# Kernel optimization log

Measured on AMD Instinct MI355X. Metric: run time of the kernel, lower is better.

Reference implementation:

```python
import jax, jax.numpy as jnp
import numpy as np

B, P, C, WIN = 64, 24, 40, 64          # batch, acoustic params, phoneme classes, window
L1 = WIN - 4                            # after conv k=5: 60
L2 = L1 - 4                             # after primary conv k=5: 56
R = P * L2                              # num_routes = 24*56 = 1344
IC, OC = 32, 16                         # capsule in/out channels
NUM_ITERS = 3


def squash(x, axis=-1):
    sq = jnp.sum(x * x, axis=axis, keepdims=True)
    return (sq / (1.0 + sq)) * x / (jnp.sqrt(sq) + 1e-8)


def conv1d(x, w, b):
    # x: (B, Cin, L), w: (Cout, Cin, K)
    out = jax.lax.conv_general_dilated(x, w, (1,), 'VALID',
                                       dimension_numbers=('NCH', 'OIH', 'NCH'))
    return out + b[None, :, None]


def batchnorm(x, g, b):
    # training-mode BN over (batch, length) per channel; x: (B, Ch, L)
    m = jnp.mean(x, axis=(0, 2), keepdims=True)
    v = jnp.var(x, axis=(0, 2), keepdims=True)
    return g[None, :, None] * (x - m) / jnp.sqrt(v + 1e-5) + b[None, :, None]


def setup_inputs() -> dict:
    key = jax.random.key(0)
    ks = jax.random.split(key, 12)
    d = {}
    d['x'] = jax.random.normal(ks[0], (B, WIN, P), dtype=jnp.float32)
    # project: Conv1d(24 -> 256, k=5) + BN(256)
    d['conv1_w'] = jax.random.normal(ks[1], (256, P, 5), dtype=jnp.float32) * (1.0 / np.sqrt(P * 5))
    d['conv1_b'] = jnp.zeros((256,), dtype=jnp.float32)
    d['bn1_g'] = jnp.ones((256,), dtype=jnp.float32)
    d['bn1_b'] = jnp.zeros((256,), dtype=jnp.float32)
    d['prim_w'] = jax.random.normal(ks[2], (P * 32, 256, 5), dtype=jnp.float32) * (1.0 / np.sqrt(256 * 5))
    d['prim_b'] = jnp.zeros((P * 32,), dtype=jnp.float32)
    d['bn2_g'] = jnp.ones((32,), dtype=jnp.float32)
    d['bn2_b'] = jnp.zeros((32,), dtype=jnp.float32)
    # digit capsule routing weights (1, C, R, 16, 32) as in torch (randn)
    d['W_cap'] = jax.random.normal(ks[3], (1, C, R, OC, IC), dtype=jnp.float32) * 0.05
    # classifier: Linear(16*C -> 256), Linear(256 -> C)
    d['cls_w1'] = jax.random.normal(ks[4], (256, OC * C), dtype=jnp.float32) * (1.0 / np.sqrt(OC * C))
    d['cls_b1'] = jnp.zeros((256,), dtype=jnp.float32)
    d['cls_w2'] = jax.random.normal(ks[5], (C, 256), dtype=jnp.float32) * (1.0 / np.sqrt(256))
    d['cls_b2'] = jnp.zeros((C,), dtype=jnp.float32)
    d['dec_w1'] = jax.random.normal(ks[6], (256, OC * C), dtype=jnp.float32) * (1.0 / np.sqrt(OC * C))
    d['dec_b1'] = jnp.zeros((256,), dtype=jnp.float32)
    d['dec_w2'] = jax.random.normal(ks[7], (WIN * P, 256), dtype=jnp.float32) * (1.0 / np.sqrt(256))
    d['dec_b2'] = jnp.zeros((WIN * P,), dtype=jnp.float32)
    return d


def reference(x, conv1_w, conv1_b, bn1_g, bn1_b, prim_w, prim_b, bn2_g, bn2_b,
              W_cap, cls_w1, cls_b1, cls_w2, cls_b2, dec_w1, dec_b1, dec_w2, dec_b2):
    h = jax.nn.relu(batchnorm(conv1d(jnp.transpose(x, (0, 2, 1)), conv1_w, conv1_b), bn1_g, bn1_b))
    # primary capsules: fused conv -> (B, 24*32, 56); capsule i occupies length slice i
    u = conv1d(h, prim_w, prim_b)                       # (B, 768, 56)
    u = u.reshape(B, P, 32, L2).transpose(0, 2, 1, 3).reshape(B, 32, R)  # concat along length dim
    u = batchnorm(u, bn2_g, bn2_b)
    u = squash(jnp.transpose(u, (0, 2, 1)), axis=-1)    # (B, R, 32)
    # digit capsule: u_hat = W @ x  -> (B, C, R, 16)
    u_hat = jnp.einsum('crdi,bri->bcrd', W_cap[0], u)
    # dynamic routing
    b_ij = jnp.zeros((B, C, R, 1), dtype=u_hat.dtype)
    for it in range(NUM_ITERS):
        c_ij = jax.nn.softmax(b_ij, axis=1)             # softmax over capsules
        s_j = jnp.sum(c_ij * u_hat, axis=2)             # (B, C, 16)
        v_j = squash(s_j, axis=-1)
        if it < NUM_ITERS - 1:
            a_ij = jnp.einsum('bcrd,bcd->bcr', u_hat, v_j)[..., None]
            b_ij = b_ij + a_ij
    flat = v_j.reshape(B, -1)                           # (B, 640)
    logits = jax.nn.relu(flat @ cls_w1.T + cls_b1) @ cls_w2.T + cls_b2
    pred_y = jax.nn.softmax(logits, axis=-1)
    # y is None branch: one-hot of argmax
    y = jax.nn.one_hot(jnp.argmax(pred_y, axis=1), C, dtype=v_j.dtype)
    masked = (v_j * y[:, :, None]).reshape(B, -1)
    pred_x = jax.nn.sigmoid(jax.nn.relu(masked @ dec_w1.T + dec_b1) @ dec_w2.T + dec_b2)
    pred_x = pred_x.reshape(B, WIN, P)
    return (pred_x, pred_y)
```

## Files before the change

kernel.cpp:

```cpp
#include <hip/hip_runtime.h>
#include <math.h>

#define BB_ 64
#define P_  24
#define C_  40
#define WIN_ 64
#define L1_ 60
#define L2_ 56
#define R_  1344

#define O_USQ   0ull
#define O_UHAT  2752512ull
#define O_H     30277632ull
#define O_HB    3735552ull
#define O_WT    4227072ull
#define O_UP    25755648ull
#define O_HID   31260672ull
#define O_HD    31277056ull
#define O_STATS 57802752ull
#define O_A1    57803328ull
#define O_B1S   57803584ull
#define O_A2    57803840ull
#define O_B2S   57803872ull
#define O_S     57803904ull
#define O_V     57967744ull
#define WS_FLOATS_NEEDED 58008704ull

typedef short bf16x8 __attribute__((ext_vector_type(8)));
typedef float f32x4 __attribute__((ext_vector_type(4)));

__device__ __forceinline__ float dot4f(float4 a, float4 b) {
    return a.x*b.x + a.y*b.y + a.z*b.z + a.w*b.w;
}

__device__ __forceinline__ unsigned short f2bf(float x) {
    unsigned int u = __float_as_uint(x);
    u += 0x7fffu + ((u >> 16) & 1u);
    return (unsigned short)(u >> 16);
}
__device__ __forceinline__ float bfl(unsigned int u) {
    return __uint_as_float(u << 16);
}
__device__ __forceinline__ float bfh(unsigned int u) {
    return __uint_as_float(u & 0xffff0000u);
}

__global__ void k0w(const float* __restrict__ w2, unsigned short* __restrict__ wt) {
    int o2 = blockIdx.x, t = threadIdx.x;
    const float* src = &w2[(size_t)o2 * 1280 + t * 5];
    #pragma unroll
    for (int kt = 0; kt < 5; kt++)
        wt[((size_t)kt * 768 + o2) * 256 + t] = f2bf(src[kt]);
}

__global__ void k1_conv1(const float* __restrict__ x, const float* __restrict__ w1,
                         const float* __restrict__ c1b, float* __restrict__ h) {
    __shared__ float xs[24 * 20];
    __shared__ float wl[64 * 121];
    int t = threadIdx.x;
    int lq = blockIdx.x, b = blockIdx.y, ocg = blockIdx.z;
    for (int idx = t; idx < 456; idx += 256) {
        int p = idx / 19, tau = idx - p * 19;
        xs[p * 20 + tau] = x[b * 1536 + (lq * 15 + tau) * 24 + p];
    }
    for (int idx = t; idx < 7680; idx += 256) {
        int o_ = idx / 120, cix = idx - o_ * 120;
        wl[o_ * 121 + cix] = w1[(ocg * 64 + o_) * 120 + cix];
    }
    __syncthreads();
    int g = t >> 6;
    int ol = t & 63;
    int LV = (g < 3) ? 4 : 3;
    int o = ocg * 64 + ol;
    float acc[4] = {0.f, 0.f, 0.f, 0.f};
    for (int p = 0; p < 24; p++) {
        float4 xa = *(const float4*)&xs[p * 20 + g * 4];
        float4 xb = *(const float4*)&xs[p * 20 + g * 4 + 4];
        float xr[8] = {xa.x, xa.y, xa.z, xa.w, xb.x, xb.y, xb.z, xb.w};
        #pragma unroll
        for (int k = 0; k < 5; k++) {
            float w = wl[ol * 121 + p * 5 + k];
            #pragma unroll
            for (int li = 0; li < 4; li++) acc[li] += xr[li + k] * w;
        }
    }
    for (int li = 0; li < LV; li++) {
        int l = lq * 15 + g * 4 + li;
        h[(size_t)(b * 60 + l) * 256 + o] = acc[li] + c1b[o];
    }
}

__global__ void k2a(const float* __restrict__ h, float* __restrict__ sum1, float* __restrict__ ss1) {
    int t = threadIdx.x;
    float s = 0.f, q = 0.f;
    for (int i = 0; i < 64; i++) {
        float v = h[(size_t)(blockIdx.x * 64 + i) * 256 + t];
        s += v; q += v * v;
    }
    atomicAdd(&sum1[t], s);
    atomicAdd(&ss1[t], q);
}

__global__ void k2b(const float* __restrict__ sum1, const float* __restrict__ ss1,
                    const float* __restrict__ g, const float* __restrict__ be,
                    float* __restrict__ a1, float* __restrict__ b1s) {
    int o = threadIdx.x;
    float m = sum1[o] * (1.f / 3840.f);
    float v = ss1[o] * (1.f / 3840.f) - m * m;
    float a = g[o] / sqrtf(v + 1e-5f);
    a1[o] = a;
    b1s[o] = be[o] - m * a;
}

__global__ void k2c(const float* __restrict__ h, const float* __restrict__ a1,
                    const float* __restrict__ b1s, unsigned short* __restrict__ hb) {
    int gid = blockIdx.x * 256 + threadIdx.x;
    int base = gid * 4;
    int ic = base & 255;
    float4 v = *(const float4*)&h[base];
    float4 a = *(const float4*)&a1[ic];
    float4 bb = *(const float4*)&b1s[ic];
    unsigned int w0 = (unsigned int)f2bf(fmaxf(v.x * a.x + bb.x, 0.f))
                    | ((unsigned int)f2bf(fmaxf(v.y * a.y + bb.y, 0.f)) << 16);
    unsigned int w1 = (unsigned int)f2bf(fmaxf(v.z * a.z + bb.z, 0.f))
                    | ((unsigned int)f2bf(fmaxf(v.w * a.w + bb.w, 0.f)) << 16);
    uint2 o = {w0, w1};
    *(uint2*)&hb[base] = o;
}

__global__ __launch_bounds__(256) void k3_mfma(
        const unsigned short* __restrict__ hb, const unsigned short* __restrict__ wt,
        const float* __restrict__ pb, float* __restrict__ up) {
    __shared__ unsigned short hs[68 * 40];
    __shared__ unsigned short wsd[5 * 64 * 40];
    int t = threadIdx.x;
    int m0 = blockIdx.x * 64;
    int b = blockIdx.y;
    int wid = t >> 6, lane = t & 63;
    int wm = wid >> 1, wn = wid & 1;
    int ln = lane & 15, grp = lane >> 4;

    f32x4 acc[2][2];
    #pragma unroll
    for (int i = 0; i < 2; i++)
        #pragma unroll
        for (int j = 0; j < 2; j++) acc[i][j] = (f32x4){0.f, 0.f, 0.f, 0.f};

    for (int ic0 = 0; ic0 < 256; ic0 += 32) {
        __syncthreads();
        for (int idx = t; idx < 272; idx += 256) {
            int row = idx >> 2, q = idx & 3;
            int hrow = row < 60 ? row : 59;
            uint4 v = *(const uint4*)&hb[((size_t)b * 60 + hrow) * 256 + ic0 + q * 8];
            *(uint4*)&hs[row * 40 + q * 8] = v;
        }
        #pragma unroll
        for (int it = 0; it < 5; it++) {
            int idx = it * 256 + t;
            int row = idx >> 2, q = idx & 3;
            int kt = row >> 6, o2l = row & 63;
            uint4 v = *(const uint4*)&wt[((size_t)kt * 768 + m0 + o2l) * 256 + ic0 + q * 8];
            *(uint4*)&wsd[row * 40 + q * 8] = v;
        }
        __syncthreads();
        #pragma unroll
        for (int kt = 0; kt < 5; kt++) {
            bf16x8 af0 = *(const bf16x8*)&wsd[(kt * 64 + wm * 32 + ln) * 40 + grp * 8];
            bf16x8 af1 = *(const bf16x8*)&wsd[(kt * 64 + wm * 32 + 16 + ln) * 40 + grp * 8];
            bf16x8 bf0 = *(const bf16x8*)&hs[(wn * 32 + ln + kt) * 40 + grp * 8];
            bf16x8 bf1 = *(const bf16x8*)&hs[(wn * 32 + 16 + ln + kt) * 40 + grp * 8];
            acc[0][0] = __builtin_amdgcn_mfma_f32_16x16x32_bf16(af0, bf0, acc[0][0], 0, 0, 0);
            acc[0][1] = __builtin_amdgcn_mfma_f32_16x16x32_bf16(af0, bf1, acc[0][1], 0, 0, 0);
            acc[1][0] = __builtin_amdgcn_mfma_f32_16x16x32_bf16(af1, bf0, acc[1][0], 0, 0, 0);
            acc[1][1] = __builtin_amdgcn_mfma_f32_16x16x32_bf16(af1, bf1, acc[1][1], 0, 0, 0);
        }
    }
    #pragma unroll
    for (int ms = 0; ms < 2; ms++) {
        int o2 = m0 + wm * 32 + ms * 16 + grp * 4;
        float4 pv = *(const float4*)&pb[o2];
        #pragma unroll
        for (int ns = 0; ns < 2; ns++) {
            int l = wn * 32 + ns * 16 + ln;
            if (l < 56) {
                float4 v;
                v.x = acc[ms][ns][0] + pv.x;
                v.y = acc[ms][ns][1] + pv.y;
                v.z = acc[ms][ns][2] + pv.z;
                v.w = acc[ms][ns][3] + pv.w;
                *(float4*)&up[(size_t)b * 43008 + (size_t)l * 768 + o2] = v;
            }
        }
    }
}

__global__ void k4s(const float* __restrict__ up, float* __restrict__ sum2, float* __restrict__ ss2) {
    __shared__ float rs[256], rq[256];
    int t = threadIdx.x;
    float s = 0.f, q = 0.f;
    for (int i = 0; i < 32; i++) {
        size_t row = (size_t)(blockIdx.x * 32 + i) * 768;
        for (int c0 = 0; c0 < 768; c0 += 256) {
            float v = up[row + c0 + t];
            s += v; q += v * v;
        }
    }
    rs[t] = s; rq[t] = q;
    __syncthreads();
    if (t < 32) {
        float S = 0.f, Q = 0.f;
        for (int g2 = 0; g2 < 8; g2++) { S += rs[t + 32 * g2]; Q += rq[t + 32 * g2]; }
        atomicAdd(&sum2[t], S);
        atomicAdd(&ss2[t], Q);
    }
}

__global__ void k4b(const float* __restrict__ sum2, const float* __restrict__ ss2,
                    const float* __restrict__ g, const float* __restrict__ be,
                    float* __restrict__ a2, float* __restrict__ b2s) {
    int j = threadIdx.x;
    if (j >= 32) return;
    float m = sum2[j] * (1.f / 86016.f);
    float v = ss2[j] * (1.f / 86016.f) - m * m;
    float a = g[j] / sqrtf(v + 1e-5f);
    a2[j] = a;
    b2s[j] = be[j] - m * a;
}

__global__ void k5(const float* __restrict__ up, const float* __restrict__ a2,
                   const float* __restrict__ b2s, float* __restrict__ usq) {
    int t = threadIdx.x;
    int row = blockIdx.x * 8 + (t >> 5);
    int j = t & 31;
    int b = row / 1344, r = row - b * 1344;
    int p = r / 56, l = r - p * 56;
    float v = up[(size_t)b * 43008 + (size_t)l * 768 + p * 32 + j];
    float xv = a2[j] * v + b2s[j];
    float sq = xv * xv;
    #pragma unroll
    for (int m = 16; m >= 1; m >>= 1) sq += __shfl_xor(sq, m, 32);
    float scale = (sq / (1.f + sq)) / (sqrtf(sq) + 1e-8f);
    usq[(size_t)row * 32 + j] = xv * scale;
}

__global__ __launch_bounds__(256) void k6_uhat(const float* __restrict__ usq,
                                               const float* __restrict__ W,
                                               unsigned short* __restrict__ uhb) {
    __shared__ float us[64 * 36];
    __shared__ float wl[128 * 36];
    int t = threadIdx.x;
    int cdt = blockIdx.x, r = blockIdx.y;

    #pragma unroll
    for (int q = 0; q < 2; q++) {
        int idx4 = q * 256 + t;
        int b = idx4 >> 3, i4 = idx4 & 7;
        float4 v = *(const float4*)&usq[(size_t)(b * 1344 + r) * 32 + i4 * 4];
        *(float4*)&us[b * 36 + i4 * 4] = v;
    }
    #pragma unroll
    for (int q = 0; q < 4; q++) {
        int idx4 = q * 256 + t;
        int c_l = idx4 >> 7;
        int rest4 = idx4 & 127;
        float4 v = *(const float4*)&W[(size_t)(cdt * 8 + c_l) * 688128ull +
                                      (size_t)r * 512 + rest4 * 4];
        int cd_l = c_l * 16 + (rest4 >> 3);
        int i4 = rest4 & 7;
        *(float4*)&wl[cd_l * 36 + i4 * 4] = v;
    }
    __syncthreads();

    int tb = t & 7, tcd = t >> 3;
    float acc[8][4];
    #pragma unroll
    for (int i = 0; i < 8; i++)
        #pragma unroll
        for (int j = 0; j < 4; j++) acc[i][j] = 0.f;

    #pragma unroll
    for (int k4 = 0; k4 < 8; k4++) {
        float4 wv[4], ub[8];
        #pragma unroll
        for (int j = 0; j < 4; j++)
            wv[j] = *(const float4*)&wl[(tcd * 4 + j) * 36 + k4 * 4];
        #pragma unroll
        for (int bj = 0; bj < 8; bj++)
            ub[bj] = *(const float4*)&us[(bj * 8 + tb) * 36 + k4 * 4];
        #pragma unroll
        for (int bj = 0; bj < 8; bj++)
            #pragma unroll
            for (int j = 0; j < 4; j++)
                acc[bj][j] += dot4f(ub[bj], wv[j]);
    }

    #pragma unroll
    for (int bj = 0; bj < 8; bj++) {
        int b = bj * 8 + tb;
        unsigned int lo = (unsigned int)f2bf(acc[bj][0]) | ((unsigned int)f2bf(acc[bj][1]) << 16);
        unsigned int hi = (unsigned int)f2bf(acc[bj][2]) | ((unsigned int)f2bf(acc[bj][3]) << 16);
        uint2 o = {lo, hi};
        *(uint2*)&uhb[(size_t)(b * 1344 + r) * 640 + cdt * 128 + tcd * 4] = o;
    }
}

template<int UNIFORM>
__global__ void k_route(const unsigned short* __restrict__ uhb, const float* __restrict__ vsum,
                        float* __restrict__ sout) {
    __shared__ float sl[2560];
    int t = threadIdx.x, wid = t >> 6, lane = t & 63;
    int b = blockIdx.y, rt = blockIdx.x;
    bool act = lane < 40;
    int c = act ? lane : 0;
    float4 vs0 = {0,0,0,0}, vs1 = vs0, vs2 = vs0, vs3 = vs0;
    if (UNIFORM == 0 && act) {
        const float4* vp = (const float4*)&vsum[b * 640 + c * 16];
        vs0 = vp[0]; vs1 = vp[1]; vs2 = vp[2]; vs3 = vp[3];
    }
    float4 ac0 = {0,0,0,0}, ac1 = ac0, ac2 = ac0, ac3 = ac0;
    for (int i = 0; i < 8; i++) {
        int r = rt * 32 + wid * 8 + i;
        const uint4* u4 = (const uint4*)&uhb[((size_t)(b * 1344 + r) * 40 + c) * 16];
        float4 a0 = {0,0,0,0}, a1 = a0, a2 = a0, a3 = a0;
        if (act) {
            uint4 q0 = u4[0], q1 = u4[1];
            a0.x = bfl(q0.x); a0.y = bfh(q0.x); a0.z = bfl(q0.y); a0.w = bfh(q0.y);
            a1.x = bfl(q0.z); a1.y = bfh(q0.z); a1.z = bfl(q0.w); a1.w = bfh(q0.w);
            a2.x = bfl(q1.x); a2.y = bfh(q1.x); a2.z = bfl(q1.y); a2.w = bfh(q1.y);
            a3.x = bfl(q1.z); a3.y = bfh(q1.z); a3.z = bfl(q1.w); a3.w = bfh(q1.w);
        }
        float w;
        if (UNIFORM) {
            w = 0.025f;
        } else {
            float dt = act ? (dot4f(a0, vs0) + dot4f(a1, vs1) + dot4f(a2, vs2) + dot4f(a3, vs3))
                           : -1e30f;
            float mx = dt;
            #pragma unroll
            for (int m2 = 32; m2 >= 1; m2 >>= 1) mx = fmaxf(mx, __shfl_xor(mx, m2));
            float e = act ? __expf(dt - mx) : 0.f;
            float se = e;
            #pragma unroll
            for (int m2 = 32; m2 >= 1; m2 >>= 1) se += __shfl_xor(se, m2);
            w = e / se;
        }
        ac0.x += w * a0.x; ac0.y += w * a0.y; ac0.z += w * a0.z; ac0.w += w * a0.w;
        ac1.x += w * a1.x; ac1.y += w * a1.y; ac1.z += w * a1.z; ac1.w += w * a1.w;
        ac2.x += w * a2.x; ac2.y += w * a2.y; ac2.z += w * a2.z; ac2.w += w * a2.w;
        ac3.x += w * a3.x; ac3.y += w * a3.y; ac3.z += w * a3.z; ac3.w += w * a3.w;
    }
    if (act) {
        float4* sp = (float4*)&sl[wid * 640 + c * 16];
        sp[0] = ac0; sp[1] = ac1; sp[2] = ac2; sp[3] = ac3;
    }
    __syncthreads();
    for (int jj = t; jj < 640; jj += 256)
        atomicAdd(&sout[b * 640 + jj], sl[jj] + sl[640 + jj] + sl[1280 + jj] + sl[1920 + jj]);
}

__global__ void k8(const float* __restrict__ sin, float* __restrict__ vout,
                   float* __restrict__ vsum, int addsum) {
    int t = threadIdx.x;
    int row = blockIdx.x * 16 + (t >> 4);
    int d = t & 15;
    float v = sin[row * 16 + d];
    float sq = v * v;
    #pragma unroll
    for (int m = 8; m >= 1; m >>= 1) sq += __shfl_xor(sq, m, 16);
    float scale = (sq / (1.f + sq)) / (sqrtf(sq) + 1e-8f);
    float o = v * scale;
    vout[row * 16 + d] = o;
    if (addsum) vsum[row * 16 + d] += o;
}

__global__ void k10a(const float* __restrict__ v, const float* __restrict__ cw1,
                     const float* __restrict__ cb1, float* __restrict__ hid) {
    __shared__ float flat[640];
    int t = threadIdx.x;
    int b = blockIdx.x, hq = blockIdx.y;
    for (int j = t; j < 640; j += 256) flat[j] = v[b * 640 + j];
    __syncthreads();
    int h_l = t >> 2, s = t & 3;
    int h = hq * 64 + h_l;
    const float4* wr = (const float4*)&cw1[(size_t)h * 640 + s * 160];
    float a = 0.f;
    #pragma unroll
    for (int u = 0; u < 40; u++) {
        float4 w4 = wr[u];
        float4 f4 = *(const float4*)&flat[s * 160 + u * 4];
        a += dot4f(w4, f4);
    }
    a += __shfl_xor(a, 1);
    a += __shfl_xor(a, 2);
    if (s == 0) hid[b * 256 + h] = fmaxf(a + cb1[h], 0.f);
}

__global__ void k10bc(const float* __restrict__ v, const float* __restrict__ hid,
                      const float* __restrict__ cw2, const float* __restrict__ cb2,
                      const float* __restrict__ dw1, const float* __restrict__ db1,
                      float* __restrict__ out, float* __restrict__ hd) {
    __shared__ float hl[256], lgs[40], msk[16];
    __shared__ float smx, ssum;
    __shared__ int chat;
    int t = threadIdx.x, b = blockIdx.x;
    if (t < 256) hl[t] = hid[b * 256 + t];
    __syncthreads();
    {
        int c = t >> 3, s = t & 7;
        float p = 0.f;
        const float4* w4 = (const float4*)&cw2[c * 256 + s * 32];
        const float4* h4 = (const float4*)&hl[s * 32];
        #pragma unroll
        for (int u = 0; u < 8; u++) p += dot4f(w4[u], h4[u]);
        p += __shfl_xor(p, 1); p += __shfl_xor(p, 2); p += __shfl_xor(p, 4);
        if (s == 0) lgs[c] = p + cb2[c];
    }
    __syncthreads();
    if (t == 0) {
        float mx = lgs[0]; int am = 0;
        for (int c2 = 1; c2 < 40; c2++) if (lgs[c2] > mx) { mx = lgs[c2]; am = c2; }
        float se = 0.f;
        for (int c2 = 0; c2 < 40; c2++) se += __expf(lgs[c2] - mx);
        smx = mx; ssum = se; chat = am;
    }
    __syncthreads();
    if (t < 40) out[98304 + b * 40 + t] = __expf(lgs[t] - smx) / ssum;
    if (t < 16) msk[t] = v[b * 640 + chat * 16 + t];
    __syncthreads();
    if (t < 256) {
        int cb = chat * 16;
        float ad = db1[t];
        const float4* w4 = (const float4*)&dw1[(size_t)t * 640 + cb];
        #pragma unroll
        for (int u = 0; u < 4; u++) {
            float4 m4 = *(const float4*)&msk[u * 4];
            ad += dot4f(w4[u], m4);
        }
        hd[b * 256 + t] = fmaxf(ad, 0.f);
    }
}

__global__ void k10d(const float* __restrict__ hd, const float* __restrict__ dw2,
                     const float* __restrict__ db2, float* __restrict__ out) {
    __shared__ float hl[256];
    int t = threadIdx.x;
    int b = blockIdx.x, ot = blockIdx.y;
    if (t < 256) hl[t] = hd[b * 256 + t];
    __syncthreads();
    int o_l = t >> 2, s = t & 3;
    int o = ot * 64 + o_l;
    const float4* w4 = (const float4*)&dw2[(size_t)o * 256 + s * 64];
    const float4* h4 = (const float4*)&hl[s * 64];
    float z = 0.f;
    #pragma unroll
    for (int u = 0; u < 16; u++) z += dot4f(w4[u], h4[u]);
    z += __shfl_xor(z, 1);
    z += __shfl_xor(z, 2);
    if (s == 0) out[b * 1536 + o] = 1.f / (1.f + __expf(-(z + db2[o])));
}

extern "C" void kernel_launch(void* const* d_in, const int* in_sizes, int n_in,
                              void* d_out, int out_size, void* d_ws, size_t ws_size,
                              hipStream_t stream) {
    const float* x   = (const float*)d_in[0];
    const float* c1w = (const float*)d_in[1];
    const float* c1b = (const float*)d_in[2];
    const float* g1  = (const float*)d_in[3];
    const float* be1 = (const float*)d_in[4];
    const float* pw  = (const float*)d_in[5];
    const float* pb  = (const float*)d_in[6];
    const float* g2  = (const float*)d_in[7];
    const float* be2 = (const float*)d_in[8];
    const float* Wc  = (const float*)d_in[9];
    const float* cw1 = (const float*)d_in[10];
    const float* cb1 = (const float*)d_in[11];
    const float* cw2 = (const float*)d_in[12];
    const float* cb2 = (const float*)d_in[13];
    const float* dw1 = (const float*)d_in[14];
    const float* db1 = (const float*)d_in[15];
    const float* dw2 = (const float*)d_in[16];
    const float* db2 = (const float*)d_in[17];

    if (ws_size < WS_FLOATS_NEEDED * 4ull) return;

    float* ws  = (float*)d_ws;
    float* out = (float*)d_out;
    float* usq  = ws + O_USQ;
    unsigned short* uhb = (unsigned short*)(ws + O_UHAT);
    float* hpre = ws + O_H;
    unsigned short* hbb = (unsigned short*)(ws + O_HB);
    unsigned short* wtb = (unsigned short*)(ws + O_WT);
    float* up   = ws + O_UP;
    float* hidb = ws + O_HID;
    float* hdb  = ws + O_HD;
    float* sum1 = ws + O_STATS;
    float* ss1  = sum1 + 256;
    float* sum2 = ss1 + 256;
    float* ss2  = sum2 + 32;
    float* a1  = ws + O_A1;
    float* b1s = ws + O_B1S;
    float* a2  = ws + O_A2;
    float* b2s = ws + O_B2S;
    float* s0   = ws + O_S;
    float* s1   = s0 + 40960;
    float* s2   = s1 + 40960;
    float* vsum = s2 + 40960;
    float* vbuf = ws + O_V;

    hipMemsetAsync(sum1, 0, 576 * sizeof(float), stream);
    hipMemsetAsync(s0, 0, 163840 * sizeof(float), stream);

    k0w<<<768, 256, 0, stream>>>(pw, wtb);
    k1_conv1<<<dim3(4, 64, 4), 256, 0, stream>>>(x, c1w, c1b, hpre);
    k2a<<<60, 256, 0, stream>>>(hpre, sum1, ss1);
    k2b<<<1, 256, 0, stream>>>(sum1, ss1, g1, be1, a1, b1s);
    k2c<<<960, 256, 0, stream>>>(hpre, a1, b1s, hbb);
    k3_mfma<<<dim3(12, 64), 256, 0, stream>>>(hbb, wtb, pb, up);
    k4s<<<112, 256, 0, stream>>>(up, sum2, ss2);
    k4b<<<1, 64, 0, stream>>>(sum2, ss2, g2, be2, a2, b2s);
    k5<<<10752, 256, 0, stream>>>(up, a2, b2s, usq);
    k6_uhat<<<dim3(5, 1344), 256, 0, stream>>>(usq, Wc, uhb);
    k_route<1><<<dim3(42, 64), 256, 0, stream>>>(uhb, nullptr, s0);
    k8<<<160, 256, 0, stream>>>(s0, vbuf, vsum, 1);
    k_route<0><<<dim3(42, 64), 256, 0, stream>>>(uhb, vsum, s1);
    k8<<<160, 256, 0, stream>>>(s1, vbuf, vsum, 1);
    k_route<0><<<dim3(42, 64), 256, 0, stream>>>(uhb, vsum, s2);
    k8<<<160, 256, 0, stream>>>(s2, vbuf, vsum, 0);
    k10a<<<dim3(64, 4), 256, 0, stream>>>(vbuf, cw1, cb1, hidb);
    k10bc<<<64, 320, 0, stream>>>(vbuf, hidb, cw2, cb2, dw1, db1, out, hdb);
    k10d<<<dim3(64, 24), 256, 0, stream>>>(hdb, dw2, db2, out);
}
```

Before: 381.5 us.

## Compute u_hat with bf16 MFMA instead of scalar FP32 dot products

Replaces the FP32 FMA-based u_hat kernel with one that converts the capsule inputs and routing weights to bf16 and uses 16x16x32 MFMA instructions, with one block per route covering all 40 classes. W is read straight from global into registers with no LDS staging, and the capsule inputs are staged once in LDS as bf16. This cuts ALU work and shared-memory traffic. In exchange it adds bf16 rounding of the weights and inputs, which lowers precision.

```diff
diff --git a/kernel.cpp b/kernel.cpp
--- a/kernel.cpp
+++ b/kernel.cpp
@@ -243,64 +243,56 @@
     usq[(size_t)row * 32 + j] = xv * scale;
 }
 
-__global__ __launch_bounds__(256) void k6_uhat(const float* __restrict__ usq,
+__global__ __launch_bounds__(256) void k6_mfma(const float* __restrict__ usq,
                                                const float* __restrict__ W,
                                                unsigned short* __restrict__ uhb) {
-    __shared__ float us[64 * 36];
-    __shared__ float wl[128 * 36];
-    int t = threadIdx.x;
-    int cdt = blockIdx.x, r = blockIdx.y;
-
-    #pragma unroll
-    for (int q = 0; q < 2; q++) {
-        int idx4 = q * 256 + t;
-        int b = idx4 >> 3, i4 = idx4 & 7;
-        float4 v = *(const float4*)&usq[(size_t)(b * 1344 + r) * 32 + i4 * 4];
-        *(float4*)&us[b * 36 + i4 * 4] = v;
-    }
-    #pragma unroll
-    for (int q = 0; q < 4; q++) {
-        int idx4 = q * 256 + t;
-        int c_l = idx4 >> 7;
-        int rest4 = idx4 & 127;
-        float4 v = *(const float4*)&W[(size_t)(cdt * 8 + c_l) * 688128ull +
-                                      (size_t)r * 512 + rest4 * 4];
-        int cd_l = c_l * 16 + (rest4 >> 3);
-        int i4 = rest4 & 7;
-        *(float4*)&wl[cd_l * 36 + i4 * 4] = v;
-    }
-    __syncthreads();
-
-    int tb = t & 7, tcd = t >> 3;
-    float acc[8][4];
-    #pragma unroll
-    for (int i = 0; i < 8; i++)
-        #pragma unroll
-        for (int j = 0; j < 4; j++) acc[i][j] = 0.f;
-
-    #pragma unroll
-    for (int k4 = 0; k4 < 8; k4++) {
-        float4 wv[4], ub[8];
-        #pragma unroll
-        for (int j = 0; j < 4; j++)
-            wv[j] = *(const float4*)&wl[(tcd * 4 + j) * 36 + k4 * 4];
-        #pragma unroll
-        for (int bj = 0; bj < 8; bj++)
-            ub[bj] = *(const float4*)&us[(bj * 8 + tb) * 36 + k4 * 4];
-        #pragma unroll
-        for (int bj = 0; bj < 8; bj++)
-            #pragma unroll
-            for (int j = 0; j < 4; j++)
-                acc[bj][j] += dot4f(ub[bj], wv[j]);
-    }
-
-    #pragma unroll
-    for (int bj = 0; bj < 8; bj++) {
-        int b = bj * 8 + tb;
-        unsigned int lo = (unsigned int)f2bf(acc[bj][0]) | ((unsigned int)f2bf(acc[bj][1]) << 16);
-        unsigned int hi = (unsigned int)f2bf(acc[bj][2]) | ((unsigned int)f2bf(acc[bj][3]) << 16);
-        uint2 o = {lo, hi};
-        *(uint2*)&uhb[(size_t)(b * 1344 + r) * 640 + cdt * 128 + tcd * 4] = o;
+    __shared__ unsigned short ub[64 * 40];
+    int t = threadIdx.x;
+    int r = blockIdx.x;
+    {
+        int b = t >> 2, ch = t & 3;
+        const float* src = &usq[((size_t)b * 1344 + r) * 32 + ch * 8];
+        float4 v0 = *(const float4*)&src[0];
+        float4 v1 = *(const float4*)&src[4];
+        uint4 pk;
+        pk.x = (unsigned)f2bf(v0.x) | ((unsigned)f2bf(v0.y) << 16);
+        pk.y = (unsigned)f2bf(v0.z) | ((unsigned)f2bf(v0.w) << 16);
+        pk.z = (unsigned)f2bf(v1.x) | ((unsigned)f2bf(v1.y) << 16);
+        pk.w = (unsigned)f2bf(v1.z) | ((unsigned)f2bf(v1.w) << 16);
+        *(uint4*)&ub[b * 40 + ch * 8] = pk;
+    }
+    __syncthreads();
+    int w = t >> 6, lane = t & 63;
+    int ln = lane & 15, g = lane >> 4;
+    bf16x8 bfr[4];
+    #pragma unroll
+    for (int nt = 0; nt < 4; nt++)
+        bfr[nt] = *(const bf16x8*)&ub[(nt * 16 + ln) * 40 + g * 8];
+    #pragma unroll 2
+    for (int j = 0; j < 10; j++) {
+        int tm = j * 4 + w;
+        const float* asrc = &W[(((size_t)tm * 1344 + r) * 16 + ln) * 32 + g * 8];
+        float4 a0 = *(const float4*)&asrc[0];
+        float4 a1 = *(const float4*)&asrc[4];
+        union { bf16x8 v; unsigned int u[4]; } af;
+        af.u[0] = (unsigned)f2bf(a0.x) | ((unsigned)f2bf(a0.y) << 16);
+        af.u[1] = (unsigned)f2bf(a0.z) | ((unsigned)f2bf(a0.w) << 16);
+        af.u[2] = (unsigned)f2bf(a1.x) | ((unsigned)f2bf(a1.y) << 16);
+        af.u[3] = (unsigned)f2bf(a1.z) | ((unsigned)f2bf(a1.w) << 16);
+        f32x4 acc[4];
+        #pragma unroll
+        for (int nt = 0; nt < 4; nt++) {
+            acc[nt] = (f32x4){0.f, 0.f, 0.f, 0.f};
+            acc[nt] = __builtin_amdgcn_mfma_f32_16x16x32_bf16(af.v, bfr[nt], acc[nt], 0, 0, 0);
+        }
+        #pragma unroll
+        for (int nt = 0; nt < 4; nt++) {
+            int b = nt * 16 + ln;
+            unsigned lo = (unsigned)f2bf(acc[nt][0]) | ((unsigned)f2bf(acc[nt][1]) << 16);
+            unsigned hi = (unsigned)f2bf(acc[nt][2]) | ((unsigned)f2bf(acc[nt][3]) << 16);
+            uint2 o = {lo, hi};
+            *(uint2*)&uhb[(((size_t)b * 1344 + r) * 40 + tm) * 16 + g * 4] = o;
+        }
     }
 }
 
@@ -519,7 +511,7 @@
     k4s<<<112, 256, 0, stream>>>(up, sum2, ss2);
     k4b<<<1, 64, 0, stream>>>(sum2, ss2, g2, be2, a2, b2s);
     k5<<<10752, 256, 0, stream>>>(up, a2, b2s, usq);
-    k6_uhat<<<dim3(5, 1344), 256, 0, stream>>>(usq, Wc, uhb);
+    k6_mfma<<<1344, 256, 0, stream>>>(usq, Wc, uhb);
     k_route<1><<<dim3(42, 64), 256, 0, stream>>>(uhb, nullptr, s0);
     k8<<<160, 256, 0, stream>>>(s0, vbuf, vsum, 1);
     k_route<0><<<dim3(42, 64), 256, 0, stream>>>(uhb, vsum, s1);
```

Result: slower. 405.2 us (+6.2%).
